# Performance work log

Hardware: AMD Instinct MI355X
Metric: run time of the kernel (lower is better)

## Reference

```python
import jax, jax.numpy as jnp
import numpy as np

D = 128          # embed_dim
NB = 30          # hardcoded neighbor count in neighbor_encoder
STEPS = 4        # process_steps
NSYM = 200000    # num_symbols (pad idx = NSYM)
B = 4096         # query batch
FEW = 5          # support pairs


def setup_inputs() -> dict:
    key = jax.random.key(0)
    ks = jax.random.split(key, 32)
    g = lambda i, shape, s=0.02: jax.random.normal(ks[i], shape, dtype=jnp.float32) * s
    inp = {}
    # embedding tables (row NSYM is padding, zeros)
    inp['emb'] = g(0, (NSYM + 1, D), 0.1).at[NSYM].set(0.0)
    inp['emb_var'] = g(1, (NSYM + 1, D), 0.1).at[NSYM].set(0.0)
    # neighbor attention (mean path)
    inp['nW'], inp['nWb'] = g(2, (D, 2 * D)), jnp.zeros((D,), jnp.float32)
    inp['nu'], inp['nub'] = g(3, (1, D)), jnp.zeros((1,), jnp.float32)
    # neighbor attention (var path)
    inp['nvW'], inp['nvWb'] = g(4, (D, 2 * D)), jnp.zeros((D,), jnp.float32)
    inp['nvu'], inp['nvub'] = g(5, (1, D)), jnp.zeros((1,), jnp.float32)
    # SupportEncoder: d_model=2D, d_inner=4D
    inp['p1W'], inp['p1b'] = g(6, (4 * D, 2 * D)), jnp.zeros((4 * D,), jnp.float32)
    inp['p2W'], inp['p2b'] = g(7, (2 * D, 4 * D)), jnp.zeros((2 * D,), jnp.float32)
    inp['ln_a'], inp['ln_b'] = jnp.ones((2 * D,), jnp.float32), jnp.zeros((2 * D,), jnp.float32)
    # QueryEncoder LSTMCell: input 2D, hidden 4D (torch gate order i,f,g,o)
    inp['Wih'], inp['Whh'] = g(8, (16 * D, 2 * D)), g(9, (16 * D, 4 * D))
    inp['bih'], inp['bhh'] = jnp.zeros((16 * D,), jnp.float32), jnp.zeros((16 * D,), jnp.float32)
    # connections: (..., 0)=relation idx, (..., 1)=entity idx
    inp['q_left'] = jax.random.randint(ks[10], (B, NB, 2), 0, NSYM, dtype=jnp.int32)
    inp['q_right'] = jax.random.randint(ks[11], (B, NB, 2), 0, NSYM, dtype=jnp.int32)
    inp['s_left'] = jax.random.randint(ks[12], (FEW, NB, 2), 0, NSYM, dtype=jnp.int32)
    inp['s_right'] = jax.random.randint(ks[13], (FEW, NB, 2), 0, NSYM, dtype=jnp.int32)
    return inp


def _layer_norm(z, a, b, eps=0.001):
    # faithful to torch: std with Bessel correction (ddof=1)
    mu = jnp.mean(z, axis=-1, keepdims=True)
    sigma = jnp.std(z, axis=-1, keepdims=True, ddof=1)
    return (z - mu) / (sigma + eps) * a + b


def reference(emb, emb_var, nW, nWb, nu, nub, nvW, nvWb, nvu, nvub,
              p1W, p1b, p2W, p2b, ln_a, ln_b, Wih, Whh, bih, bhh,
              q_left, q_right, s_left, s_right):

    def neighbor_encoder(conn):
        rel, ent = conn[..., 0], conn[..., 1]
        rel_e, ent_e = emb[rel], emb[ent]                      # [N, NB, D]
        cat = jnp.concatenate([rel_e, ent_e], axis=-1)         # [N, NB, 2D]
        a = jnp.tanh(cat @ nW.T + nWb) @ nu.T + nub            # [N, NB, 1]
        att = jax.nn.softmax(a[..., 0], axis=1)                # softmax over neighbors
        out = jnp.einsum('nk,nkd->nd', att, ent_e)
        rel_v, ent_v = emb_var[rel], emb_var[ent]
        catv = jnp.concatenate([rel_v, ent_v], axis=-1)
        av = jnp.tanh(catv @ nvW.T + nvWb) @ nvu.T + nvub
        attv = jax.nn.softmax(av[..., 0], axis=1)
        out_v = jnp.einsum('nk,nkd->nd', attv, ent_e)          # torch quirk: pools ent_embeds
        return jnp.tanh(out), jnp.tanh(out_v)

    def support_encoder(x):
        h = jax.nn.relu(x @ p1W.T + p1b) @ p2W.T + p2b
        return _layer_norm(h + x, ln_a, ln_b)

    def lstm_cell(x, h, c):
        gates = x @ Wih.T + bih + h @ Whh.T + bhh
        i, f, g_, o = jnp.split(gates, 4, axis=-1)
        c = jax.nn.sigmoid(f) * c + jax.nn.sigmoid(i) * jnp.tanh(g_)
        return jax.nn.sigmoid(o) * jnp.tanh(c), c

    def query_encoder(support, query):
        n = query.shape[0]
        h_r = jnp.zeros((n, 4 * D), query.dtype)
        c = jnp.zeros((n, 4 * D), query.dtype)
        h = query
        for _ in range(STEPS):
            h_r_, c = lstm_cell(query, h_r, c)
            h = query + h_r_[:, :2 * D]
            attn = jax.nn.softmax(h @ support.T, axis=1)
            r = attn @ support
            h_r = jnp.concatenate([h, r], axis=1)
        return h

    ql, qlv = neighbor_encoder(q_left)
    qr, qrv = neighbor_encoder(q_right)
    sl, slv = neighbor_encoder(s_left)
    sr, srv = neighbor_encoder(s_right)

    query = jnp.concatenate([ql, qr], axis=-1)       # [B, 2D]
    query_v = jnp.concatenate([qlv, qrv], axis=-1)
    support = jnp.concatenate([sl, sr], axis=-1)     # [FEW, 2D]
    support_v = jnp.concatenate([slv, srv], axis=-1)

    def match(q, s):
        s_g = support_encoder(s)
        q_g = support_encoder(q)
        q_f = query_encoder(s_g, q_g)
        s_mean = jnp.mean(s_g, axis=0, keepdims=True)  # [1, 2D]
        return (q_f @ s_mean.T)[:, 0]                  # [B]

    score = match(query, support)
    score_var = match(query_v, support_v)
    return jnp.stack([score, score_var])               # [2, B]
```

## Files before the change

### kernel.cpp

```cpp
#include <hip/hip_runtime.h>
#include <math.h>

#define DD    128
#define TWOD  256
#define FOURD 512
#define NBN   30
#define BQ    4096
#define FEWN  5
#define NSYM  200000
#define KTOT  768
#define NGATE 1024
#define ULIVE 256
#define TOTU  (2 * BQ + 2 * FEWN)
#define UPB   4
#define PSTR  136

typedef short bf16x8 __attribute__((ext_vector_type(8)));
typedef float f32x4 __attribute__((ext_vector_type(4)));

__device__ __forceinline__ float sigmoidf_(float x) { return 1.0f / (1.0f + expf(-x)); }

__device__ __forceinline__ float ftanh(float x) {
    float e = __expf(2.0f * x);
    return 1.0f - 2.0f / (e + 1.0f);
}

__device__ __forceinline__ unsigned short f2bf(float f) {
    unsigned int u = __float_as_uint(f);
    unsigned int r = (u + 0x7fffu + ((u >> 16) & 1u)) >> 16;
    return (unsigned short)r;
}

__device__ __forceinline__ float bf2f(unsigned short s) {
    return __uint_as_float(((unsigned int)s) << 16);
}

__device__ __forceinline__ bf16x8 pack8(float4 a, float4 b) {
    union { bf16x8 v; unsigned int u[4]; } r;
    r.u[0] = ((__float_as_uint(a.x) + 0x8000u) >> 16) | ((__float_as_uint(a.y) + 0x8000u) & 0xffff0000u);
    r.u[1] = ((__float_as_uint(a.z) + 0x8000u) >> 16) | ((__float_as_uint(a.w) + 0x8000u) & 0xffff0000u);
    r.u[2] = ((__float_as_uint(b.x) + 0x8000u) >> 16) | ((__float_as_uint(b.y) + 0x8000u) & 0xffff0000u);
    r.u[3] = ((__float_as_uint(b.z) + 0x8000u) >> 16) | ((__float_as_uint(b.w) + 0x8000u) & 0xffff0000u);
    return r.v;
}

__device__ __forceinline__ void gload_lds16(const void* g, void* l) {
    __builtin_amdgcn_global_load_lds((const __attribute__((address_space(1))) unsigned int*)g,
                                     (__attribute__((address_space(3))) unsigned int*)l,
                                     16, 0, 0);
}

__global__ __launch_bounds__(256) void k_prep(
    const float* __restrict__ Wih, const float* __restrict__ Whh,
    const float* __restrict__ bih, const float* __restrict__ bhh,
    const float* __restrict__ p1W, const float* __restrict__ p2W,
    const float* __restrict__ nW, const float* __restrict__ nvW,
    unsigned short* __restrict__ Wbf, float* __restrict__ biasR,
    float* __restrict__ p1WT, float* __restrict__ p2WT,
    unsigned short* __restrict__ Nbf)
{
    int idx = blockIdx.x * 256 + threadIdx.x;
    int stride = gridDim.x * 256;
    for (int i = idx; i < NGATE * KTOT; i += stride) {
        int n = i / KTOT, k = i - n * KTOT;
        int blk = n >> 6, rem = n & 63;
        int g = rem >> 4, ul = rem & 15;
        int u = blk * 16 + ul;
        int srcrow = g * 512 + u;
        float v = (k < TWOD) ? Wih[srcrow * TWOD + k] : Whh[srcrow * FOURD + (k - TWOD)];
        Wbf[i] = f2bf(v);
    }
    for (int n = idx; n < NGATE; n += stride) {
        int blk = n >> 6, rem = n & 63;
        int g = rem >> 4, ul = rem & 15;
        int u = blk * 16 + ul;
        int srcrow = g * 512 + u;
        biasR[n] = bih[srcrow] + bhh[srcrow];
    }
    for (int i = idx; i < FOURD * TWOD; i += stride) {
        int o = i / TWOD, j = i % TWOD;
        p1WT[j * FOURD + o] = p1W[o * TWOD + j];
    }
    for (int i = idx; i < TWOD * FOURD; i += stride) {
        int o = i / FOURD, j = i % FOURD;
        p2WT[j * TWOD + o] = p2W[o * FOURD + j];
    }
    for (int i = idx; i < 2 * DD * TWOD; i += stride) {
        float v = (i < DD * TWOD) ? nW[i] : nvW[i - DD * TWOD];
        Nbf[i] = f2bf(v);
    }
}

__global__ __launch_bounds__(256, 2) void k_neighbor_v4(
    const float* __restrict__ emb, const float* __restrict__ emb_var,
    const unsigned short* __restrict__ Nbf,
    const float* __restrict__ nWb, const float* __restrict__ nu,
    const float* __restrict__ nvWb, const float* __restrict__ nvu,
    const int* __restrict__ q_left, const int* __restrict__ q_right,
    const int* __restrict__ s_left, const int* __restrict__ s_right,
    float* __restrict__ query, float* __restrict__ support)
{
    const int tid  = threadIdx.x;
    const int wave = tid >> 6, lane = tid & 63;
    const int quad = lane >> 4, m15 = lane & 15;
    const int pw   = wave >> 1;
    const int wn   = wave & 1;
    const int u0   = blockIdx.x * UPB;

    __shared__ __align__(16) unsigned short Sg[4 * 32 * PSTR];
    __shared__ int   sidxL[UPB][64];
    __shared__ float aP[2][2][32];
    __shared__ float attL[2][32];

    {
        int un = tid >> 6, i = tid & 63;
        int uu_ = u0 + un; if (uu_ >= TOTU) uu_ = TOTU - 1;
        const int* conn;
        if (uu_ < BQ)                 conn = q_left  + uu_ * (NBN * 2);
        else if (uu_ < 2 * BQ)        conn = q_right + (uu_ - BQ) * (NBN * 2);
        else if (uu_ < 2 * BQ + FEWN) conn = s_left  + (uu_ - 2 * BQ) * (NBN * 2);
        else                          conn = s_right + (uu_ - 2 * BQ - FEWN) * (NBN * 2);
        sidxL[un][i] = (i < NBN * 2) ? conn[i] : NSYM;
    }

    const unsigned short* Bw = Nbf + (size_t)pw * DD * TWOD;
    const float* Wb = pw ? nvWb : nWb;
    const float* uu = pw ? nvu  : nu;
    bf16x8 Bf[4][8];
    float nb[4], un_[4];
#pragma unroll
    for (int t = 0; t < 4; ++t) {
        int n = wn * 64 + t * 16 + m15;
#pragma unroll
        for (int kt = 0; kt < 8; ++kt)
            Bf[t][kt] = *(const bf16x8*)(Bw + n * TWOD + kt * 32 + quad * 8);
        nb[t] = Wb[n];
        un_[t] = uu[n];
    }
    __syncthreads();

    for (int r = 0; r < UPB; ++r) {
        const int uidx = u0 + r;

        {
            const int g = wave;
            const float* table = (g < 2) ? emb : emb_var;
            const int side = g & 1;
            const int colf = (lane & 15) * 8;
            const int rsub = lane >> 4;
#pragma unroll
            for (int i = 0; i < 8; ++i) {
                int row = i * 4 + rsub;
                int sym = sidxL[r][2 * row + side];
                const float* src = table + (size_t)sym * DD + colf;
                float4 x0 = *(const float4*)src;
                float4 x1 = *(const float4*)(src + 4);
                *(bf16x8*)&Sg[(g * 32 + row) * PSTR + colf] = pack8(x0, x1);
            }
        }
        __syncthreads();

        const int pg = pw ? 2 : 0;
        f32x4 acc[2][4] = {};
#pragma unroll
        for (int kt = 0; kt < 8; ++kt) {
            const int g = (kt < 4) ? pg : pg + 1;
            const int coff = (kt & 3) * 32 + quad * 8;
            bf16x8 fa[2];
#pragma unroll
            for (int mt = 0; mt < 2; ++mt)
                fa[mt] = *(const bf16x8*)&Sg[(g * 32 + mt * 16 + m15) * PSTR + coff];
#pragma unroll
            for (int mt = 0; mt < 2; ++mt)
#pragma unroll
                for (int nt = 0; nt < 4; ++nt)
                    acc[mt][nt] = __builtin_amdgcn_mfma_f32_16x16x32_bf16(fa[mt], Bf[nt][kt], acc[mt][nt], 0, 0, 0);
        }

        {
            float part[2][4];
#pragma unroll
            for (int mt = 0; mt < 2; ++mt)
#pragma unroll
                for (int rr = 0; rr < 4; ++rr) {
                    float s = 0.f;
#pragma unroll
                    for (int nt = 0; nt < 4; ++nt)
                        s += un_[nt] * ftanh(acc[mt][nt][rr] + nb[nt]);
                    part[mt][rr] = s;
                }
#pragma unroll
            for (int off = 1; off < 16; off <<= 1)
#pragma unroll
                for (int mt = 0; mt < 2; ++mt)
#pragma unroll
                    for (int rr = 0; rr < 4; ++rr)
                        part[mt][rr] += __shfl_xor(part[mt][rr], off, 64);
            if (m15 == 0) {
#pragma unroll
                for (int mt = 0; mt < 2; ++mt)
#pragma unroll
                    for (int rr = 0; rr < 4; ++rr)
                        aP[pw][wn][mt * 16 + quad * 4 + rr] = part[mt][rr];
            }
        }
        __syncthreads();

        if ((wave & 1) == 0 && lane < 32) {
            const int p = wave >> 1;
            float sc = (lane < NBN) ? aP[p][0][lane] + aP[p][1][lane] : -1e30f;
            float mx = sc;
#pragma unroll
            for (int off = 1; off < 32; off <<= 1) mx = fmaxf(mx, __shfl_xor(mx, off, 64));
            float e = (lane < NBN) ? __expf(sc - mx) : 0.f;
            float sum = e;
#pragma unroll
            for (int off = 1; off < 32; off <<= 1) sum += __shfl_xor(sum, off, 64);
            attL[p][lane] = e / sum;
        }
        __syncthreads();

        {
            const int p = tid >> 7;
            const int d = tid & 127;
            float pool = 0.f;
#pragma unroll
            for (int k = 0; k < NBN; ++k)
                pool += attL[p][k] * bf2f(Sg[(32 + k) * PSTR + d]);
            if (uidx < TOTU) {
                float* dst;
                if (uidx < BQ)                 dst = query   + ((size_t)p * BQ + uidx) * TWOD;
                else if (uidx < 2 * BQ)        dst = query   + ((size_t)p * BQ + (uidx - BQ)) * TWOD + DD;
                else if (uidx < 2 * BQ + FEWN) dst = support + ((size_t)p * FEWN + (uidx - 2 * BQ)) * TWOD;
                else                           dst = support + ((size_t)p * FEWN + (uidx - 2 * BQ - FEWN)) * TWOD + DD;
                dst[d] = ftanh(pool);
            }
        }
        __syncthreads();
    }
}

template <int RPB>
__global__ __launch_bounds__(256) void k_supenc(
    const float* __restrict__ xin, float* __restrict__ xout,
    unsigned short* __restrict__ abf,
    const float* __restrict__ p1WT, const float* __restrict__ p1b,
    const float* __restrict__ p2WT, const float* __restrict__ p2b,
    const float* __restrict__ ln_a, const float* __restrict__ ln_b)
{
    const int tid = threadIdx.x;
    const int r0 = blockIdx.x * RPB;
    __shared__ float X[RPB][TWOD];
    __shared__ float H1[RPB][FOURD];
    __shared__ float red[4][RPB][2];
    __shared__ float muv[RPB], sgv[RPB];

    for (int idx = tid; idx < RPB * TWOD; idx += 256) {
        int r = idx >> 8, j = idx & 255;
        X[r][j] = xin[(size_t)(r0 + r) * TWOD + j];
    }
    __syncthreads();

    {
        float acc[RPB][2] = {};
        for (int j = 0; j < TWOD; j += 4) {
            float w0[4], w1[4];
#pragma unroll
            for (int jj = 0; jj < 4; ++jj) {
                w0[jj] = p1WT[(j + jj) * FOURD + tid];
                w1[jj] = p1WT[(j + jj) * FOURD + tid + 256];
            }
#pragma unroll
            for (int r = 0; r < RPB; ++r) {
                float x[4] __attribute__((aligned(16)));
                *(float4*)x = *(const float4*)&X[r][j];
#pragma unroll
                for (int jj = 0; jj < 4; ++jj) {
                    acc[r][0] += x[jj] * w0[jj];
                    acc[r][1] += x[jj] * w1[jj];
                }
            }
        }
        float b0 = p1b[tid], b1 = p1b[tid + 256];
#pragma unroll
        for (int r = 0; r < RPB; ++r) {
            H1[r][tid]       = fmaxf(acc[r][0] + b0, 0.f);
            H1[r][tid + 256] = fmaxf(acc[r][1] + b1, 0.f);
        }
    }
    __syncthreads();

    float z[RPB];
    {
        float acc[RPB] = {};
        for (int j = 0; j < FOURD; j += 4) {
            float w[4];
#pragma unroll
            for (int jj = 0; jj < 4; ++jj) w[jj] = p2WT[(j + jj) * TWOD + tid];
#pragma unroll
            for (int r = 0; r < RPB; ++r) {
                float h[4] __attribute__((aligned(16)));
                *(float4*)h = *(const float4*)&H1[r][j];
#pragma unroll
                for (int jj = 0; jj < 4; ++jj) acc[r] += h[jj] * w[jj];
            }
        }
        float b = p2b[tid];
#pragma unroll
        for (int r = 0; r < RPB; ++r) z[r] = acc[r] + b + X[r][tid];
    }
    {
        float s[RPB], ss[RPB];
#pragma unroll
        for (int r = 0; r < RPB; ++r) { s[r] = z[r]; ss[r] = z[r] * z[r]; }
#pragma unroll
        for (int off = 1; off < 64; off <<= 1)
#pragma unroll
            for (int r = 0; r < RPB; ++r) {
                s[r]  += __shfl_xor(s[r],  off, 64);
                ss[r] += __shfl_xor(ss[r], off, 64);
            }
        const int wv = tid >> 6, lane = tid & 63;
        if (lane == 0) {
#pragma unroll
            for (int r = 0; r < RPB; ++r) { red[wv][r][0] = s[r]; red[wv][r][1] = ss[r]; }
        }
        __syncthreads();
        if (tid < RPB) {
            float st  = red[0][tid][0] + red[1][tid][0] + red[2][tid][0] + red[3][tid][0];
            float sst = red[0][tid][1] + red[1][tid][1] + red[2][tid][1] + red[3][tid][1];
            float mu  = st / (float)TWOD;
            float var = fmaxf((sst - (float)TWOD * mu * mu) / ((float)TWOD - 1.f), 0.f);
            muv[tid] = mu; sgv[tid] = sqrtf(var);
        }
        __syncthreads();
    }
#pragma unroll
    for (int r = 0; r < RPB; ++r) {
        float o = (z[r] - muv[r]) / (sgv[r] + 1e-3f) * ln_a[tid] + ln_b[tid];
        xout[(size_t)(r0 + r) * TWOD + tid] = o;
        if (abf) abf[(size_t)(r0 + r) * KTOT + tid] = f2bf(o);
    }
}

__global__ __launch_bounds__(256) void k_lstm_mfma(
    const unsigned short* __restrict__ Abf,
    const unsigned short* __restrict__ Wbf,
    const float* __restrict__ biasR,
    float* __restrict__ cst, float* __restrict__ hbuf)
{
    __shared__ __align__(16) unsigned short As[128 * 32];
    __shared__ __align__(16) unsigned short Bs[128 * 32];
    const int tid  = threadIdx.x;
    const int wave = tid >> 6, lane = tid & 63;
    const int quad = lane >> 4, m15 = lane & 15;
    const int m0 = blockIdx.x * 128;
    const int n0 = blockIdx.y * 128;
    const int wm = wave >> 1, wn = wave & 1;
    const int lrow = lane >> 2, lslot = lane & 3;

    f32x4 acc[4][4] = {};

    for (int kt = 0; kt < KTOT / 32; ++kt) {
        const int k0 = kt * 32;
        __syncthreads();
#pragma unroll
        for (int t = 0; t < 2; ++t) {
            int c = wave * 2 + t;
            int row = c * 16 + lrow;
            int kg = lslot ^ ((row >> 1) & 3);
            gload_lds16(Abf + (size_t)(m0 + row) * KTOT + k0 + kg * 8, As + c * 512);
            gload_lds16(Wbf + (size_t)(n0 + row) * KTOT + k0 + kg * 8, Bs + c * 512);
        }
        __syncthreads();

        bf16x8 fa[4], fb[4];
#pragma unroll
        for (int mi = 0; mi < 4; ++mi) {
            int ra = wm * 64 + mi * 16 + m15;
            int sa = quad ^ ((ra >> 1) & 3);
            fa[mi] = *(const bf16x8*)(As + ra * 32 + sa * 8);
            int rb = wn * 64 + mi * 16 + m15;
            int sb = quad ^ ((rb >> 1) & 3);
            fb[mi] = *(const bf16x8*)(Bs + rb * 32 + sb * 8);
        }
#pragma unroll
        for (int mi = 0; mi < 4; ++mi)
#pragma unroll
            for (int ni = 0; ni < 4; ++ni)
                acc[mi][ni] = __builtin_amdgcn_mfma_f32_16x16x32_bf16(fa[mi], fb[ni], acc[mi][ni], 0, 0, 0);
    }

    const int u = ((n0 + wn * 64) >> 2) + m15;
    float bg[4];
#pragma unroll
    for (int g = 0; g < 4; ++g) bg[g] = biasR[n0 + wn * 64 + g * 16 + m15];
#pragma unroll
    for (int mi = 0; mi < 4; ++mi) {
#pragma unroll
        for (int r = 0; r < 4; ++r) {
            int gm = m0 + wm * 64 + mi * 16 + quad * 4 + r;
            size_t cidx = (size_t)gm * ULIVE + u;
            float pi = acc[mi][0][r] + bg[0];
            float pf = acc[mi][1][r] + bg[1];
            float pg = acc[mi][2][r] + bg[2];
            float po = acc[mi][3][r] + bg[3];
            float cn = sigmoidf_(pf) * cst[cidx] + sigmoidf_(pi) * tanhf(pg);
            cst[cidx]  = cn;
            hbuf[cidx] = sigmoidf_(po) * tanhf(cn);
        }
    }
}

__global__ __launch_bounds__(256) void k_lstm_attn(
    const float* __restrict__ qg, const float* __restrict__ hbuf,
    const float* __restrict__ sg, unsigned short* __restrict__ Abf,
    float* __restrict__ hfin)
{
    const int tid = threadIdx.x;
    const int p   = blockIdx.y;
    const int wv = tid >> 6, lane = tid & 63;
    __shared__ float sgl[FEWN][TWOD];
    for (int idx = tid; idx < FEWN * TWOD; idx += 256)
        sgl[idx >> 8][idx & 255] = sg[p * FEWN * TWOD + idx];
    __syncthreads();
    const int j0 = lane * 4;
    for (int rr = 0; rr < 8; ++rr) {
        int row = blockIdx.x * 32 + wv * 8 + rr;
        size_t g = (size_t)p * BQ + row;
        float4 q4 = *(const float4*)(qg + g * TWOD + j0);
        float4 t4 = *(const float4*)(hbuf + g * ULIVE + j0);
        float h[4] __attribute__((aligned(16))) = {q4.x + t4.x, q4.y + t4.y, q4.z + t4.z, q4.w + t4.w};
        float sv[FEWN][4] __attribute__((aligned(16)));
        float pa[FEWN];
#pragma unroll
        for (int f = 0; f < FEWN; ++f) {
            *(float4*)sv[f] = *(const float4*)&sgl[f][j0];
            pa[f] = h[0] * sv[f][0] + h[1] * sv[f][1] + h[2] * sv[f][2] + h[3] * sv[f][3];
        }
#pragma unroll
        for (int off = 1; off < 64; off <<= 1)
#pragma unroll
            for (int f = 0; f < FEWN; ++f) pa[f] += __shfl_xor(pa[f], off, 64);
        float mx = pa[0];
#pragma unroll
        for (int f = 1; f < FEWN; ++f) mx = fmaxf(mx, pa[f]);
        float sum = 0.f, e[FEWN];
#pragma unroll
        for (int f = 0; f < FEWN; ++f) { e[f] = expf(pa[f] - mx); sum += e[f]; }
        float inv = 1.f / sum;
        float r4[4] __attribute__((aligned(16))) = {0.f, 0.f, 0.f, 0.f};
#pragma unroll
        for (int f = 0; f < FEWN; ++f) {
            float a = e[f] * inv;
#pragma unroll
            for (int q = 0; q < 4; ++q) r4[q] += a * sv[f][q];
        }
        unsigned short tb[4] __attribute__((aligned(8)));
#pragma unroll
        for (int q = 0; q < 4; ++q) tb[q] = f2bf(h[q]);
        *(uint2*)(Abf + g * KTOT + TWOD + j0) = *(uint2*)tb;
#pragma unroll
        for (int q = 0; q < 4; ++q) tb[q] = f2bf(r4[q]);
        *(uint2*)(Abf + g * KTOT + FOURD + j0) = *(uint2*)tb;
        *(float4*)(hfin + g * TWOD + j0) = *(float4*)h;
    }
}

__global__ __launch_bounds__(256) void k_score(
    const float* __restrict__ hfin, const float* __restrict__ sg, float* __restrict__ out)
{
    const int tid = threadIdx.x;
    const int p   = blockIdx.y;
    __shared__ float sm[TWOD];
    if (tid < TWOD) {
        const float* s = sg + p * FEWN * TWOD + tid;
        sm[tid] = (s[0] + s[TWOD] + s[2 * TWOD] + s[3 * TWOD] + s[4 * TWOD]) / 5.0f;
    }
    __syncthreads();
    const int wv = tid >> 6, lane = tid & 63;
    const int j0 = lane * 4;
    for (int rr = 0; rr < 8; ++rr) {
        int row = blockIdx.x * 32 + wv * 8 + rr;
        const float* h = hfin + ((size_t)p * BQ + row) * TWOD + j0;
        float4 h4 = *(const float4*)h;
        float4 s4 = *(const float4*)&sm[j0];
        float pv = h4.x * s4.x + h4.y * s4.y + h4.z * s4.z + h4.w * s4.w;
#pragma unroll
        for (int off = 1; off < 64; off <<= 1) pv += __shfl_xor(pv, off, 64);
        if (lane == 0) out[p * BQ + row] = pv;
    }
}

extern "C" void kernel_launch(void* const* d_in, const int* in_sizes, int n_in,
                              void* d_out, int out_size, void* d_ws, size_t ws_size,
                              hipStream_t stream)
{
    const float* emb     = (const float*)d_in[0];
    const float* emb_var = (const float*)d_in[1];
    const float* nW      = (const float*)d_in[2];
    const float* nWb     = (const float*)d_in[3];
    const float* nu      = (const float*)d_in[4];
    const float* nub     = (const float*)d_in[5];
    const float* nvW     = (const float*)d_in[6];
    const float* nvWb    = (const float*)d_in[7];
    const float* nvu     = (const float*)d_in[8];
    const float* nvub    = (const float*)d_in[9];
    const float* p1W     = (const float*)d_in[10];
    const float* p1b     = (const float*)d_in[11];
    const float* p2W     = (const float*)d_in[12];
    const float* p2b     = (const float*)d_in[13];
    const float* ln_a    = (const float*)d_in[14];
    const float* ln_b    = (const float*)d_in[15];
    const float* Wih     = (const float*)d_in[16];
    const float* Whh     = (const float*)d_in[17];
    const float* bih     = (const float*)d_in[18];
    const float* bhh     = (const float*)d_in[19];
    const int* q_left    = (const int*)d_in[20];
    const int* q_right   = (const int*)d_in[21];
    const int* s_left    = (const int*)d_in[22];
    const int* s_right   = (const int*)d_in[23];

    float* ws = (float*)d_ws;
    size_t o = 0;
    float* p1WT     = ws + o; o += FOURD * TWOD;
    float* p2WT     = ws + o; o += FOURD * TWOD;
    float* biasR    = ws + o; o += NGATE;
    float* query    = ws + o; o += (size_t)2 * BQ * TWOD;
    float* supportB = ws + o; o += 2 * FEWN * TWOD;
    float* qg       = ws + o; o += (size_t)2 * BQ * TWOD;
    float* sg       = ws + o; o += 2 * FEWN * TWOD;
    float* cst      = ws + o; o += (size_t)2 * BQ * ULIVE;
    float* hbuf     = ws + o; o += (size_t)2 * BQ * ULIVE;
    unsigned short* Wbf = (unsigned short*)(ws + o); o += (size_t)NGATE * KTOT / 2;
    unsigned short* Abf = (unsigned short*)(ws + o); o += (size_t)2 * BQ * KTOT / 2;
    unsigned short* Nbf = (unsigned short*)(ws + o); o += (size_t)2 * DD * TWOD / 2;
    float* hfin     = query;

    hipMemsetAsync(cst, 0, (size_t)2 * BQ * ULIVE * sizeof(float), stream);
    hipMemsetAsync(Abf, 0, (size_t)2 * BQ * KTOT * sizeof(unsigned short), stream);

    k_prep<<<dim3(1024), dim3(256), 0, stream>>>(Wih, Whh, bih, bhh, p1W, p2W, nW, nvW,
                                                 Wbf, biasR, p1WT, p2WT, Nbf);
    k_neighbor_v4<<<dim3((TOTU + UPB - 1) / UPB), dim3(256), 0, stream>>>(
        emb, emb_var, Nbf, nWb, nu, nvWb, nvu,
        q_left, q_right, s_left, s_right, query, supportB);
    k_supenc<8><<<dim3(2 * BQ / 8), dim3(256), 0, stream>>>(query, qg, Abf, p1WT, p1b, p2WT, p2b, ln_a, ln_b);
    k_supenc<1><<<dim3(2 * FEWN), dim3(256), 0, stream>>>(supportB, sg, (unsigned short*)nullptr,
                                                          p1WT, p1b, p2WT, p2b, ln_a, ln_b);
    for (int s = 0; s < 4; ++s) {
        k_lstm_mfma<<<dim3(2 * BQ / 128, NGATE / 128), dim3(256), 0, stream>>>(Abf, Wbf, biasR, cst, hbuf);
        k_lstm_attn<<<dim3(BQ / 32, 2), dim3(256), 0, stream>>>(qg, hbuf, sg, Abf, hfin);
    }
    k_score<<<dim3(BQ / 32, 2), dim3(256), 0, stream>>>(hfin, sg, (float*)d_out);
}
```

Measured before the change: 610.1 us.

## Move support encoder to bf16 MFMA GEMMs and hoist LSTM input projection

Replaces the scalar fp32 support-encoder kernel with two bf16 MFMA GEMM kernels, the second fusing residual add and layer norm, over query and support rows stacked into one padded matrix. The loop-invariant input-to-gate projection is computed once, stored transposed in bf16, and loaded as the accumulator seed in each LSTM step, which shrinks the per-step K from 768 to 512. The neighbor kernel also prefetches the next unit's embedding rows into registers while the current unit computes. This trades extra bf16 rounding in the support encoder and a precomputed gate buffer for much less scalar FLOP work and smaller per-step GEMMs.

```diff
diff --git a/kernel.cpp b/kernel.cpp
--- a/kernel.cpp
+++ b/kernel.cpp
@@ -8,10 +8,11 @@
 #define BQ    4096
 #define FEWN  5
 #define NSYM  200000
-#define KTOT  768
 #define NGATE 1024
 #define ULIVE 256
 #define TOTU  (2 * BQ + 2 * FEWN)
+#define MQ    8192
+#define MPAD  8320
 #define UPB   4
 #define PSTR  136
 
@@ -50,55 +51,80 @@
                                      16, 0, 0);
 }
 
+template <int ROWS>
+__device__ __forceinline__ void stage_tile(const unsigned short* __restrict__ g, int stride,
+                                           int k0, unsigned short* lds, int tid) {
+#pragma unroll
+    for (int it = 0; it < (ROWS * 4) / 256; ++it) {
+        int s = it * 256 + tid;
+        int row = s >> 2, slot = s & 3;
+        int kg = slot ^ ((row >> 1) & 3);
+        gload_lds16(g + (size_t)row * stride + k0 + kg * 8, lds + s * 8);
+    }
+}
+
+__device__ __forceinline__ bf16x8 frag(const unsigned short* lds, int row, int quad) {
+    int slot = quad ^ ((row >> 1) & 3);
+    return *(const bf16x8*)(lds + row * 32 + slot * 8);
+}
+
 __global__ __launch_bounds__(256) void k_prep(
     const float* __restrict__ Wih, const float* __restrict__ Whh,
     const float* __restrict__ bih, const float* __restrict__ bhh,
     const float* __restrict__ p1W, const float* __restrict__ p2W,
     const float* __restrict__ nW, const float* __restrict__ nvW,
-    unsigned short* __restrict__ Wbf, float* __restrict__ biasR,
-    float* __restrict__ p1WT, float* __restrict__ p2WT,
+    unsigned short* __restrict__ Wqbf, unsigned short* __restrict__ Whrbf,
+    float* __restrict__ biasR,
+    unsigned short* __restrict__ p1Wbf, unsigned short* __restrict__ p2Wbf,
     unsigned short* __restrict__ Nbf)
 {
     int idx = blockIdx.x * 256 + threadIdx.x;
     int stride = gridDim.x * 256;
-    for (int i = idx; i < NGATE * KTOT; i += stride) {
-        int n = i / KTOT, k = i - n * KTOT;
+    for (int i = idx; i < NGATE * TWOD; i += stride) {
+        int n = i >> 8, k = i & 255;
         int blk = n >> 6, rem = n & 63;
         int g = rem >> 4, ul = rem & 15;
-        int u = blk * 16 + ul;
-        int srcrow = g * 512 + u;
-        float v = (k < TWOD) ? Wih[srcrow * TWOD + k] : Whh[srcrow * FOURD + (k - TWOD)];
-        Wbf[i] = f2bf(v);
+        int srcrow = g * 512 + blk * 16 + ul;
+        Wqbf[i] = f2bf(Wih[srcrow * TWOD + k]);
+    }
+    for (int i = idx; i < NGATE * FOURD; i += stride) {
+        int n = i >> 9, k = i & 511;
+        int blk = n >> 6, rem = n & 63;
+        int g = rem >> 4, ul = rem & 15;
+        int srcrow = g * 512 + blk * 16 + ul;
+        Whrbf[i] = f2bf(Whh[srcrow * FOURD + k]);
     }
     for (int n = idx; n < NGATE; n += stride) {
         int blk = n >> 6, rem = n & 63;
         int g = rem >> 4, ul = rem & 15;
-        int u = blk * 16 + ul;
-        int srcrow = g * 512 + u;
+        int srcrow = g * 512 + blk * 16 + ul;
         biasR[n] = bih[srcrow] + bhh[srcrow];
     }
-    for (int i = idx; i < FOURD * TWOD; i += stride) {
-        int o = i / TWOD, j = i % TWOD;
-        p1WT[j * FOURD + o] = p1W[o * TWOD + j];
-    }
-    for (int i = idx; i < TWOD * FOURD; i += stride) {
-        int o = i / FOURD, j = i % FOURD;
-        p2WT[j * TWOD + o] = p2W[o * FOURD + j];
-    }
-    for (int i = idx; i < 2 * DD * TWOD; i += stride) {
-        float v = (i < DD * TWOD) ? nW[i] : nvW[i - DD * TWOD];
-        Nbf[i] = f2bf(v);
-    }
-}
-
-__global__ __launch_bounds__(256, 2) void k_neighbor_v4(
+    for (int i = idx; i < FOURD * TWOD; i += stride) p1Wbf[i] = f2bf(p1W[i]);
+    for (int i = idx; i < TWOD * FOURD; i += stride) p2Wbf[i] = f2bf(p2W[i]);
+    for (int i = idx; i < 2 * DD * TWOD; i += stride)
+        Nbf[i] = f2bf((i < DD * TWOD) ? nW[i] : nvW[i - DD * TWOD]);
+}
+
+__device__ __forceinline__ void nb_issue(const float* __restrict__ table, const int* sidxr,
+                                         int side, int colf, int rsub, float4 (*pf)[2]) {
+#pragma unroll
+    for (int i = 0; i < 8; ++i) {
+        int row = i * 4 + rsub;
+        const float* src = table + (size_t)sidxr[2 * row + side] * DD + colf;
+        pf[i][0] = *(const float4*)src;
+        pf[i][1] = *(const float4*)(src + 4);
+    }
+}
+
+__global__ __launch_bounds__(256, 2) void k_neighbor_v5(
     const float* __restrict__ emb, const float* __restrict__ emb_var,
     const unsigned short* __restrict__ Nbf,
     const float* __restrict__ nWb, const float* __restrict__ nu,
     const float* __restrict__ nvWb, const float* __restrict__ nvu,
     const int* __restrict__ q_left, const int* __restrict__ q_right,
     const int* __restrict__ s_left, const int* __restrict__ s_right,
-    float* __restrict__ query, float* __restrict__ support)
+    float* __restrict__ XF, unsigned short* __restrict__ Xbf)
 {
     const int tid  = threadIdx.x;
     const int wave = tid >> 6, lane = tid & 63;
@@ -139,26 +165,24 @@
     }
     __syncthreads();
 
+    const float* table = (wave < 2) ? emb : emb_var;
+    const int side = wave & 1;
+    const int colf = (lane & 15) * 8;
+    const int rsub = lane >> 4;
+
+    float4 pf[8][2];
+    nb_issue(table, sidxL[0], side, colf, rsub, pf);
+
     for (int r = 0; r < UPB; ++r) {
         const int uidx = u0 + r;
 
-        {
-            const int g = wave;
-            const float* table = (g < 2) ? emb : emb_var;
-            const int side = g & 1;
-            const int colf = (lane & 15) * 8;
-            const int rsub = lane >> 4;
-#pragma unroll
-            for (int i = 0; i < 8; ++i) {
-                int row = i * 4 + rsub;
-                int sym = sidxL[r][2 * row + side];
-                const float* src = table + (size_t)sym * DD + colf;
-                float4 x0 = *(const float4*)src;
-                float4 x1 = *(const float4*)(src + 4);
-                *(bf16x8*)&Sg[(g * 32 + row) * PSTR + colf] = pack8(x0, x1);
-            }
-        }
-        __syncthreads();
+#pragma unroll
+        for (int i = 0; i < 8; ++i)
+            *(bf16x8*)&Sg[(wave * 32 + i * 4 + rsub) * PSTR + colf] = pack8(pf[i][0], pf[i][1]);
+        __syncthreads();
+
+        if (r + 1 < UPB)
+            nb_issue(table, sidxL[r + 1], side, colf, rsub, pf);
 
         const int pg = pw ? 2 : 0;
         f32x4 acc[2][4] = {};
@@ -228,161 +252,43 @@
             for (int k = 0; k < NBN; ++k)
                 pool += attL[p][k] * bf2f(Sg[(32 + k) * PSTR + d]);
             if (uidx < TOTU) {
-                float* dst;
-                if (uidx < BQ)                 dst = query   + ((size_t)p * BQ + uidx) * TWOD;
-                else if (uidx < 2 * BQ)        dst = query   + ((size_t)p * BQ + (uidx - BQ)) * TWOD + DD;
-                else if (uidx < 2 * BQ + FEWN) dst = support + ((size_t)p * FEWN + (uidx - 2 * BQ)) * TWOD;
-                else                           dst = support + ((size_t)p * FEWN + (uidx - 2 * BQ - FEWN)) * TWOD + DD;
-                dst[d] = ftanh(pool);
+                size_t m; int coloff;
+                if (uidx < BQ)                 { m = (size_t)p * BQ + uidx;                coloff = 0; }
+                else if (uidx < 2 * BQ)        { m = (size_t)p * BQ + (uidx - BQ);         coloff = DD; }
+                else if (uidx < 2 * BQ + FEWN) { m = MQ + p * FEWN + (uidx - 2 * BQ);      coloff = 0; }
+                else                           { m = MQ + p * FEWN + (uidx - 2 * BQ - FEWN); coloff = DD; }
+                float v = ftanh(pool);
+                XF[m * TWOD + coloff + d]  = v;
+                Xbf[m * TWOD + coloff + d] = f2bf(v);
             }
         }
         __syncthreads();
     }
 }
 
-template <int RPB>
-__global__ __launch_bounds__(256) void k_supenc(
-    const float* __restrict__ xin, float* __restrict__ xout,
-    unsigned short* __restrict__ abf,
-    const float* __restrict__ p1WT, const float* __restrict__ p1b,
-    const float* __restrict__ p2WT, const float* __restrict__ p2b,
-    const float* __restrict__ ln_a, const float* __restrict__ ln_b)
-{
-    const int tid = threadIdx.x;
-    const int r0 = blockIdx.x * RPB;
-    __shared__ float X[RPB][TWOD];
-    __shared__ float H1[RPB][FOURD];
-    __shared__ float red[4][RPB][2];
-    __shared__ float muv[RPB], sgv[RPB];
-
-    for (int idx = tid; idx < RPB * TWOD; idx += 256) {
-        int r = idx >> 8, j = idx & 255;
-        X[r][j] = xin[(size_t)(r0 + r) * TWOD + j];
-    }
-    __syncthreads();
-
-    {
-        float acc[RPB][2] = {};
-        for (int j = 0; j < TWOD; j += 4) {
-            float w0[4], w1[4];
-#pragma unroll
-            for (int jj = 0; jj < 4; ++jj) {
-                w0[jj] = p1WT[(j + jj) * FOURD + tid];
-                w1[jj] = p1WT[(j + jj) * FOURD + tid + 256];
-            }
-#pragma unroll
-            for (int r = 0; r < RPB; ++r) {
-                float x[4] __attribute__((aligned(16)));
-                *(float4*)x = *(const float4*)&X[r][j];
-#pragma unroll
-                for (int jj = 0; jj < 4; ++jj) {
-                    acc[r][0] += x[jj] * w0[jj];
-                    acc[r][1] += x[jj] * w1[jj];
-                }
-            }
-        }
-        float b0 = p1b[tid], b1 = p1b[tid + 256];
-#pragma unroll
-        for (int r = 0; r < RPB; ++r) {
-            H1[r][tid]       = fmaxf(acc[r][0] + b0, 0.f);
-            H1[r][tid + 256] = fmaxf(acc[r][1] + b1, 0.f);
-        }
-    }
-    __syncthreads();
-
-    float z[RPB];
-    {
-        float acc[RPB] = {};
-        for (int j = 0; j < FOURD; j += 4) {
-            float w[4];
-#pragma unroll
-            for (int jj = 0; jj < 4; ++jj) w[jj] = p2WT[(j + jj) * TWOD + tid];
-#pragma unroll
-            for (int r = 0; r < RPB; ++r) {
-                float h[4] __attribute__((aligned(16)));
-                *(float4*)h = *(const float4*)&H1[r][j];
-#pragma unroll
-                for (int jj = 0; jj < 4; ++jj) acc[r] += h[jj] * w[jj];
-            }
-        }
-        float b = p2b[tid];
-#pragma unroll
-        for (int r = 0; r < RPB; ++r) z[r] = acc[r] + b + X[r][tid];
-    }
-    {
-        float s[RPB], ss[RPB];
-#pragma unroll
-        for (int r = 0; r < RPB; ++r) { s[r] = z[r]; ss[r] = z[r] * z[r]; }
-#pragma unroll
-        for (int off = 1; off < 64; off <<= 1)
-#pragma unroll
-            for (int r = 0; r < RPB; ++r) {
-                s[r]  += __shfl_xor(s[r],  off, 64);
-                ss[r] += __shfl_xor(ss[r], off, 64);
-            }
-        const int wv = tid >> 6, lane = tid & 63;
-        if (lane == 0) {
-#pragma unroll
-            for (int r = 0; r < RPB; ++r) { red[wv][r][0] = s[r]; red[wv][r][1] = ss[r]; }
-        }
-        __syncthreads();
-        if (tid < RPB) {
-            float st  = red[0][tid][0] + red[1][tid][0] + red[2][tid][0] + red[3][tid][0];
-            float sst = red[0][tid][1] + red[1][tid][1] + red[2][tid][1] + red[3][tid][1];
-            float mu  = st / (float)TWOD;
-            float var = fmaxf((sst - (float)TWOD * mu * mu) / ((float)TWOD - 1.f), 0.f);
-            muv[tid] = mu; sgv[tid] = sqrtf(var);
-        }
-        __syncthreads();
-    }
-#pragma unroll
-    for (int r = 0; r < RPB; ++r) {
-        float o = (z[r] - muv[r]) / (sgv[r] + 1e-3f) * ln_a[tid] + ln_b[tid];
-        xout[(size_t)(r0 + r) * TWOD + tid] = o;
-        if (abf) abf[(size_t)(r0 + r) * KTOT + tid] = f2bf(o);
-    }
-}
-
-__global__ __launch_bounds__(256) void k_lstm_mfma(
-    const unsigned short* __restrict__ Abf,
-    const unsigned short* __restrict__ Wbf,
-    const float* __restrict__ biasR,
-    float* __restrict__ cst, float* __restrict__ hbuf)
+__global__ __launch_bounds__(256) void k_gemm_h1(
+    const unsigned short* __restrict__ Xbf, const unsigned short* __restrict__ p1Wbf,
+    const float* __restrict__ p1b, unsigned short* __restrict__ H1bf)
 {
     __shared__ __align__(16) unsigned short As[128 * 32];
     __shared__ __align__(16) unsigned short Bs[128 * 32];
-    const int tid  = threadIdx.x;
+    const int tid = threadIdx.x;
     const int wave = tid >> 6, lane = tid & 63;
     const int quad = lane >> 4, m15 = lane & 15;
-    const int m0 = blockIdx.x * 128;
-    const int n0 = blockIdx.y * 128;
+    const int m0 = blockIdx.x * 128, n0 = blockIdx.y * 128;
     const int wm = wave >> 1, wn = wave & 1;
-    const int lrow = lane >> 2, lslot = lane & 3;
 
     f32x4 acc[4][4] = {};
-
-    for (int kt = 0; kt < KTOT / 32; ++kt) {
-        const int k0 = kt * 32;
-        __syncthreads();
-#pragma unroll
-        for (int t = 0; t < 2; ++t) {
-            int c = wave * 2 + t;
-            int row = c * 16 + lrow;
-            int kg = lslot ^ ((row >> 1) & 3);
-            gload_lds16(Abf + (size_t)(m0 + row) * KTOT + k0 + kg * 8, As + c * 512);
-            gload_lds16(Wbf + (size_t)(n0 + row) * KTOT + k0 + kg * 8, Bs + c * 512);
-        }
-        __syncthreads();
-
+    for (int kt = 0; kt < 8; ++kt) {
+        __syncthreads();
+        stage_tile<128>(Xbf + (size_t)m0 * TWOD, TWOD, kt * 32, As, tid);
+        stage_tile<128>(p1Wbf + (size_t)n0 * TWOD, TWOD, kt * 32, Bs, tid);
+        __syncthreads();
         bf16x8 fa[4], fb[4];
 #pragma unroll
-        for (int mi = 0; mi < 4; ++mi) {
-            int ra = wm * 64 + mi * 16 + m15;
-            int sa = quad ^ ((ra >> 1) & 3);
-            fa[mi] = *(const bf16x8*)(As + ra * 32 + sa * 8);
-            int rb = wn * 64 + mi * 16 + m15;
-            int sb = quad ^ ((rb >> 1) & 3);
-            fb[mi] = *(const bf16x8*)(Bs + rb * 32 + sb * 8);
+        for (int i = 0; i < 4; ++i) {
+            fa[i] = frag(As, wm * 64 + i * 16 + m15, quad);
+            fb[i] = frag(Bs, wn * 64 + i * 16 + m15, quad);
         }
 #pragma unroll
         for (int mi = 0; mi < 4; ++mi)
@@ -390,45 +296,223 @@
             for (int ni = 0; ni < 4; ++ni)
                 acc[mi][ni] = __builtin_amdgcn_mfma_f32_16x16x32_bf16(fa[mi], fb[ni], acc[mi][ni], 0, 0, 0);
     }
-
+#pragma unroll
+    for (int ni = 0; ni < 4; ++ni) {
+        int col = n0 + wn * 64 + ni * 16 + m15;
+        float b = p1b[col];
+#pragma unroll
+        for (int mi = 0; mi < 4; ++mi)
+#pragma unroll
+            for (int r = 0; r < 4; ++r) {
+                int gm = m0 + wm * 64 + mi * 16 + quad * 4 + r;
+                H1bf[(size_t)gm * FOURD + col] = f2bf(fmaxf(acc[mi][ni][r] + b, 0.f));
+            }
+    }
+}
+
+__global__ __launch_bounds__(256) void k_gemm_g_ln(
+    const unsigned short* __restrict__ H1bf, const unsigned short* __restrict__ p2Wbf,
+    const float* __restrict__ p2b, const float* __restrict__ XF,
+    const float* __restrict__ ln_a, const float* __restrict__ ln_b,
+    float* __restrict__ GF, unsigned short* __restrict__ Gbf)
+{
+    __shared__ __align__(16) unsigned short As[64 * 32];
+    __shared__ __align__(16) unsigned short Bs[256 * 32];
+    __shared__ float redS[4][64], redQ[4][64];
+    const int tid = threadIdx.x;
+    const int wave = tid >> 6, lane = tid & 63;
+    const int quad = lane >> 4, m15 = lane & 15;
+    const int m0 = blockIdx.x * 64;
+    const int wn = wave;
+
+    f32x4 acc[4][4] = {};
+    for (int kt = 0; kt < 16; ++kt) {
+        __syncthreads();
+        stage_tile<64>(H1bf + (size_t)m0 * FOURD, FOURD, kt * 32, As, tid);
+        stage_tile<256>(p2Wbf, FOURD, kt * 32, Bs, tid);
+        __syncthreads();
+        bf16x8 fa[4], fb[4];
+#pragma unroll
+        for (int i = 0; i < 4; ++i) {
+            fa[i] = frag(As, i * 16 + m15, quad);
+            fb[i] = frag(Bs, wn * 64 + i * 16 + m15, quad);
+        }
+#pragma unroll
+        for (int mi = 0; mi < 4; ++mi)
+#pragma unroll
+            for (int ni = 0; ni < 4; ++ni)
+                acc[mi][ni] = __builtin_amdgcn_mfma_f32_16x16x32_bf16(fa[mi], fb[ni], acc[mi][ni], 0, 0, 0);
+    }
+#pragma unroll
+    for (int ni = 0; ni < 4; ++ni) {
+        int col = wn * 64 + ni * 16 + m15;
+        float b = p2b[col];
+#pragma unroll
+        for (int mi = 0; mi < 4; ++mi)
+#pragma unroll
+            for (int r = 0; r < 4; ++r) {
+                int gm = m0 + mi * 16 + quad * 4 + r;
+                acc[mi][ni][r] += b + XF[(size_t)gm * TWOD + col];
+            }
+    }
+#pragma unroll
+    for (int mi = 0; mi < 4; ++mi)
+#pragma unroll
+        for (int r = 0; r < 4; ++r) {
+            float s = acc[mi][0][r] + acc[mi][1][r] + acc[mi][2][r] + acc[mi][3][r];
+            float q = acc[mi][0][r] * acc[mi][0][r] + acc[mi][1][r] * acc[mi][1][r]
+                    + acc[mi][2][r] * acc[mi][2][r] + acc[mi][3][r] * acc[mi][3][r];
+#pragma unroll
+            for (int off = 1; off < 16; off <<= 1) {
+                s += __shfl_xor(s, off, 64);
+                q += __shfl_xor(q, off, 64);
+            }
+            if (m15 == 0) {
+                redS[wn][mi * 16 + quad * 4 + r] = s;
+                redQ[wn][mi * 16 + quad * 4 + r] = q;
+            }
+        }
+    __syncthreads();
+#pragma unroll
+    for (int mi = 0; mi < 4; ++mi)
+#pragma unroll
+        for (int r = 0; r < 4; ++r) {
+            int row = mi * 16 + quad * 4 + r;
+            float st = redS[0][row] + redS[1][row] + redS[2][row] + redS[3][row];
+            float sq = redQ[0][row] + redQ[1][row] + redQ[2][row] + redQ[3][row];
+            float mu = st / 256.f;
+            float var = fmaxf((sq - 256.f * mu * mu) / 255.f, 0.f);
+            float inv = 1.f / (sqrtf(var) + 1e-3f);
+            int gm = m0 + row;
+#pragma unroll
+            for (int ni = 0; ni < 4; ++ni) {
+                int col = wn * 64 + ni * 16 + m15;
+                float o = (acc[mi][ni][r] - mu) * inv * ln_a[col] + ln_b[col];
+                GF[(size_t)gm * TWOD + col]  = o;
+                Gbf[(size_t)gm * TWOD + col] = f2bf(o);
+            }
+        }
+}
+
+__global__ __launch_bounds__(256) void k_gemm_gq0(
+    const unsigned short* __restrict__ Gbf, const unsigned short* __restrict__ Wqbf,
+    unsigned short* __restrict__ gq0T)
+{
+    __shared__ __align__(16) unsigned short As[128 * 32];
+    __shared__ __align__(16) unsigned short Bs[128 * 32];
+    const int tid = threadIdx.x;
+    const int wave = tid >> 6, lane = tid & 63;
+    const int quad = lane >> 4, m15 = lane & 15;
+    const int m0 = blockIdx.x * 128, n0 = blockIdx.y * 128;
+    const int wm = wave >> 1, wn = wave & 1;
+
+    f32x4 acc[4][4] = {};
+    for (int kt = 0; kt < 8; ++kt) {
+        __syncthreads();
+        stage_tile<128>(Gbf + (size_t)m0 * TWOD, TWOD, kt * 32, As, tid);
+        stage_tile<128>(Wqbf + (size_t)n0 * TWOD, TWOD, kt * 32, Bs, tid);
+        __syncthreads();
+        bf16x8 fa[4], fb[4];
+#pragma unroll
+        for (int i = 0; i < 4; ++i) {
+            fa[i] = frag(As, wm * 64 + i * 16 + m15, quad);
+            fb[i] = frag(Bs, wn * 64 + i * 16 + m15, quad);
+        }
+#pragma unroll
+        for (int mi = 0; mi < 4; ++mi)
+#pragma unroll
+            for (int ni = 0; ni < 4; ++ni)
+                acc[mi][ni] = __builtin_amdgcn_mfma_f32_16x16x32_bf16(fa[mi], fb[ni], acc[mi][ni], 0, 0, 0);
+    }
+#pragma unroll
+    for (int ni = 0; ni < 4; ++ni) {
+        int col = n0 + wn * 64 + ni * 16 + m15;
+#pragma unroll
+        for (int mi = 0; mi < 4; ++mi) {
+            unsigned short tb[4] __attribute__((aligned(8)));
+#pragma unroll
+            for (int r = 0; r < 4; ++r) tb[r] = f2bf(acc[mi][ni][r]);
+            int gm = m0 + wm * 64 + mi * 16 + quad * 4;
+            *(uint2*)(gq0T + (size_t)col * MQ + gm) = *(uint2*)tb;
+        }
+    }
+}
+
+__global__ __launch_bounds__(256) void k_lstm_step(
+    const unsigned short* __restrict__ Abf, const unsigned short* __restrict__ Whrbf,
+    const unsigned short* __restrict__ gq0T, const float* __restrict__ biasR,
+    float* __restrict__ cst, float* __restrict__ hbuf)
+{
+    __shared__ __align__(16) unsigned short As[128 * 32];
+    __shared__ __align__(16) unsigned short Bs[128 * 32];
+    const int tid = threadIdx.x;
+    const int wave = tid >> 6, lane = tid & 63;
+    const int quad = lane >> 4, m15 = lane & 15;
+    const int m0 = blockIdx.x * 128, n0 = blockIdx.y * 128;
+    const int wm = wave >> 1, wn = wave & 1;
+
+    f32x4 acc[4][4];
+#pragma unroll
+    for (int ni = 0; ni < 4; ++ni) {
+        int col = n0 + wn * 64 + ni * 16 + m15;
+        float b = biasR[col];
+#pragma unroll
+        for (int mi = 0; mi < 4; ++mi) {
+            int gm = m0 + wm * 64 + mi * 16 + quad * 4;
+            uint2 u = *(const uint2*)(gq0T + (size_t)col * MQ + gm);
+            unsigned short* us = (unsigned short*)&u;
+#pragma unroll
+            for (int r = 0; r < 4; ++r) acc[mi][ni][r] = bf2f(us[r]) + b;
+        }
+    }
+    for (int kt = 0; kt < 16; ++kt) {
+        __syncthreads();
+        stage_tile<128>(Abf + (size_t)m0 * FOURD, FOURD, kt * 32, As, tid);
+        stage_tile<128>(Whrbf + (size_t)n0 * FOURD, FOURD, kt * 32, Bs, tid);
+        __syncthreads();
+        bf16x8 fa[4], fb[4];
+#pragma unroll
+        for (int i = 0; i < 4; ++i) {
+            fa[i] = frag(As, wm * 64 + i * 16 + m15, quad);
+            fb[i] = frag(Bs, wn * 64 + i * 16 + m15, quad);
+        }
+#pragma unroll
+        for (int mi = 0; mi < 4; ++mi)
+#pragma unroll
+            for (int ni = 0; ni < 4; ++ni)
+                acc[mi][ni] = __builtin_amdgcn_mfma_f32_16x16x32_bf16(fa[mi], fb[ni], acc[mi][ni], 0, 0, 0);
+    }
     const int u = ((n0 + wn * 64) >> 2) + m15;
-    float bg[4];
-#pragma unroll
-    for (int g = 0; g < 4; ++g) bg[g] = biasR[n0 + wn * 64 + g * 16 + m15];
 #pragma unroll
     for (int mi = 0; mi < 4; ++mi) {
 #pragma unroll
         for (int r = 0; r < 4; ++r) {
             int gm = m0 + wm * 64 + mi * 16 + quad * 4 + r;
             size_t cidx = (size_t)gm * ULIVE + u;
-            float pi = acc[mi][0][r] + bg[0];
-            float pf = acc[mi][1][r] + bg[1];
-            float pg = acc[mi][2][r] + bg[2];
-            float po = acc[mi][3][r] + bg[3];
-            float cn = sigmoidf_(pf) * cst[cidx] + sigmoidf_(pi) * tanhf(pg);
+            float cn = sigmoidf_(acc[mi][1][r]) * cst[cidx]
+                     + sigmoidf_(acc[mi][0][r]) * tanhf(acc[mi][2][r]);
             cst[cidx]  = cn;
-            hbuf[cidx] = sigmoidf_(po) * tanhf(cn);
+            hbuf[cidx] = sigmoidf_(acc[mi][3][r]) * tanhf(cn);
         }
     }
 }
 
 __global__ __launch_bounds__(256) void k_lstm_attn(
-    const float* __restrict__ qg, const float* __restrict__ hbuf,
-    const float* __restrict__ sg, unsigned short* __restrict__ Abf,
-    float* __restrict__ hfin)
+    const float* __restrict__ GF, const float* __restrict__ hbuf,
+    unsigned short* __restrict__ Abf, float* __restrict__ hfin)
 {
     const int tid = threadIdx.x;
     const int p   = blockIdx.y;
     const int wv = tid >> 6, lane = tid & 63;
     __shared__ float sgl[FEWN][TWOD];
     for (int idx = tid; idx < FEWN * TWOD; idx += 256)
-        sgl[idx >> 8][idx & 255] = sg[p * FEWN * TWOD + idx];
+        sgl[idx >> 8][idx & 255] = GF[(size_t)(MQ + p * FEWN) * TWOD + idx];
     __syncthreads();
     const int j0 = lane * 4;
     for (int rr = 0; rr < 8; ++rr) {
         int row = blockIdx.x * 32 + wv * 8 + rr;
         size_t g = (size_t)p * BQ + row;
-        float4 q4 = *(const float4*)(qg + g * TWOD + j0);
+        float4 q4 = *(const float4*)(GF + g * TWOD + j0);
         float4 t4 = *(const float4*)(hbuf + g * ULIVE + j0);
         float h[4] __attribute__((aligned(16))) = {q4.x + t4.x, q4.y + t4.y, q4.z + t4.z, q4.w + t4.w};
         float sv[FEWN][4] __attribute__((aligned(16)));
@@ -459,22 +543,22 @@
         unsigned short tb[4] __attribute__((aligned(8)));
 #pragma unroll
         for (int q = 0; q < 4; ++q) tb[q] = f2bf(h[q]);
-        *(uint2*)(Abf + g * KTOT + TWOD + j0) = *(uint2*)tb;
+        *(uint2*)(Abf + g * FOURD + j0) = *(uint2*)tb;
 #pragma unroll
         for (int q = 0; q < 4; ++q) tb[q] = f2bf(r4[q]);
-        *(uint2*)(Abf + g * KTOT + FOURD + j0) = *(uint2*)tb;
+        *(uint2*)(Abf + g * FOURD + TWOD + j0) = *(uint2*)tb;
         *(float4*)(hfin + g * TWOD + j0) = *(float4*)h;
     }
 }
 
 __global__ __launch_bounds__(256) void k_score(
-    const float* __restrict__ hfin, const float* __restrict__ sg, float* __restrict__ out)
+    const float* __restrict__ hfin, const float* __restrict__ GF, float* __restrict__ out)
 {
     const int tid = threadIdx.x;
     const int p   = blockIdx.y;
     __shared__ float sm[TWOD];
     if (tid < TWOD) {
-        const float* s = sg + p * FEWN * TWOD + tid;
+        const float* s = GF + (size_t)(MQ + p * FEWN) * TWOD + tid;
         sm[tid] = (s[0] + s[TWOD] + s[2 * TWOD] + s[3 * TWOD] + s[4 * TWOD]) / 5.0f;
     }
     __syncthreads();
@@ -523,34 +607,39 @@
 
     float* ws = (float*)d_ws;
     size_t o = 0;
-    float* p1WT     = ws + o; o += FOURD * TWOD;
-    float* p2WT     = ws + o; o += FOURD * TWOD;
-    float* biasR    = ws + o; o += NGATE;
-    float* query    = ws + o; o += (size_t)2 * BQ * TWOD;
-    float* supportB = ws + o; o += 2 * FEWN * TWOD;
-    float* qg       = ws + o; o += (size_t)2 * BQ * TWOD;
-    float* sg       = ws + o; o += 2 * FEWN * TWOD;
-    float* cst      = ws + o; o += (size_t)2 * BQ * ULIVE;
-    float* hbuf     = ws + o; o += (size_t)2 * BQ * ULIVE;
-    unsigned short* Wbf = (unsigned short*)(ws + o); o += (size_t)NGATE * KTOT / 2;
-    unsigned short* Abf = (unsigned short*)(ws + o); o += (size_t)2 * BQ * KTOT / 2;
-    unsigned short* Nbf = (unsigned short*)(ws + o); o += (size_t)2 * DD * TWOD / 2;
-    float* hfin     = query;
-
-    hipMemsetAsync(cst, 0, (size_t)2 * BQ * ULIVE * sizeof(float), stream);
-    hipMemsetAsync(Abf, 0, (size_t)2 * BQ * KTOT * sizeof(unsigned short), stream);
+    unsigned short* Wqbf  = (unsigned short*)(ws + o); o += (size_t)NGATE * TWOD / 2;
+    unsigned short* Whrbf = (unsigned short*)(ws + o); o += (size_t)NGATE * FOURD / 2;
+    float* biasR          = ws + o; o += NGATE;
+    unsigned short* p1Wbf = (unsigned short*)(ws + o); o += (size_t)FOURD * TWOD / 2;
+    unsigned short* p2Wbf = (unsigned short*)(ws + o); o += (size_t)TWOD * FOURD / 2;
+    unsigned short* Nbf   = (unsigned short*)(ws + o); o += (size_t)2 * DD * TWOD / 2;
+    float* XF             = ws + o; o += (size_t)MPAD * TWOD;
+    float* GF             = ws + o; o += (size_t)MPAD * TWOD;
+    unsigned short* Gbf   = (unsigned short*)(ws + o); o += (size_t)MPAD * TWOD / 2;
+    float* cst            = ws + o; o += (size_t)MQ * ULIVE;
+    float* hbuf           = ws + o; o += (size_t)MQ * ULIVE;
+    unsigned short* Abf   = (unsigned short*)(ws + o); o += (size_t)MQ * FOURD / 2;
+    size_t regionStart = o;
+    unsigned short* Xbf   = (unsigned short*)(ws + regionStart);
+    unsigned short* H1bf  = (unsigned short*)(ws + regionStart + (size_t)MPAD * TWOD / 2);
+    unsigned short* gq0T  = (unsigned short*)(ws + regionStart);
+    o += (size_t)NGATE * MQ / 2;
+    float* hfin = XF;
+
+    hipMemsetAsync(cst, 0, (size_t)MQ * ULIVE * sizeof(float), stream);
+    hipMemsetAsync(Abf, 0, (size_t)MQ * FOURD * sizeof(unsigned short), stream);
 
     k_prep<<<dim3(1024), dim3(256), 0, stream>>>(Wih, Whh, bih, bhh, p1W, p2W, nW, nvW,
-                                                 Wbf, biasR, p1WT, p2WT, Nbf);
-    k_neighbor_v4<<<dim3((TOTU + UPB - 1) / UPB), dim3(256), 0, stream>>>(
+                                                 Wqbf, Whrbf, biasR, p1Wbf, p2Wbf, Nbf);
+    k_neighbor_v5<<<dim3((TOTU + UPB - 1) / UPB), dim3(256), 0, stream>>>(
         emb, emb_var, Nbf, nWb, nu, nvWb, nvu,
-        q_left, q_right, s_left, s_right, query, supportB);
-    k_supenc<8><<<dim3(2 * BQ / 8), dim3(256), 0, stream>>>(query, qg, Abf, p1WT, p1b, p2WT, p2b, ln_a, ln_b);
-    k_supenc<1><<<dim3(2 * FEWN), dim3(256), 0, stream>>>(supportB, sg, (unsigned short*)nullptr,
-                                                          p1WT, p1b, p2WT, p2b, ln_a, ln_b);
+        q_left, q_right, s_left, s_right, XF, Xbf);
+    k_gemm_h1<<<dim3(MPAD / 128, 4), dim3(256), 0, stream>>>(Xbf, p1Wbf, p1b, H1bf);
+    k_gemm_g_ln<<<dim3(MPAD / 64), dim3(256), 0, stream>>>(H1bf, p2Wbf, p2b, XF, ln_a, ln_b, GF, Gbf);
+    k_gemm_gq0<<<dim3(MQ / 128, NGATE / 128), dim3(256), 0, stream>>>(Gbf, Wqbf, gq0T);
     for (int s = 0; s < 4; ++s) {
-        k_lstm_mfma<<<dim3(2 * BQ / 128, NGATE / 128), dim3(256), 0, stream>>>(Abf, Wbf, biasR, cst, hbuf);
-        k_lstm_attn<<<dim3(BQ / 32, 2), dim3(256), 0, stream>>>(qg, hbuf, sg, Abf, hfin);
-    }
-    k_score<<<dim3(BQ / 32, 2), dim3(256), 0, stream>>>(hfin, sg, (float*)d_out);
-}
+        k_lstm_step<<<dim3(MQ / 128, NGATE / 128), dim3(256), 0, stream>>>(Abf, Whrbf, gq0T, biasR, cst, hbuf);
+        k_lstm_attn<<<dim3(BQ / 32, 2), dim3(256), 0, stream>>>(GF, hbuf, Abf, hfin);
+    }
+    k_score<<<dim3(BQ / 32, 2), dim3(256), 0, stream>>>(hfin, GF, (float*)d_out);
+}
```

Result: slower. 633.9 us (+3.9%).
